# Kernel optimization log

Hardware: AMD Instinct MI355X
Metric: run time of the kernel (lower is better)

Reference implementation:

```python
import jax, jax.numpy as jnp
import numpy as np

D, H, KV, HD, F = 2048, 16, 4, 128, 5632
WIN, NG = 512, 64          # sliding window size, num global tokens
EPS = 1e-6
KEEP_ATTN = 1.0 - 0.82     # Ramanujan sparsity on attention projections
KEEP_FFN = 1.0 - 0.88      # Ramanujan sparsity on FFN projections


def _mask_w(key, shape, keep):
    """Fixed structured-sparse weight: dense init * binary keep-mask."""
    k1, k2 = jax.random.split(key)
    w = jax.random.normal(k1, shape, dtype=jnp.float32) * (shape[0] ** -0.5)
    m = (jax.random.uniform(k2, shape) < keep).astype(jnp.float32)
    return w * m


def setup_inputs() -> dict:
    key = jax.random.key(0)
    ks = jax.random.split(key, 8)
    x = jax.random.normal(ks[0], (1, 2048, D), dtype=jnp.float32)
    return {
        "x": x,
        "g_attn": jnp.ones((D,), jnp.float32),   # RMSNorm weight (attn)
        "g_ffn": jnp.ones((D,), jnp.float32),    # RMSNorm weight (ffn)
        "wq": _mask_w(ks[1], (D, H * HD), KEEP_ATTN),
        "wk": _mask_w(ks[2], (D, KV * HD), KEEP_ATTN),
        "wv": _mask_w(ks[3], (D, KV * HD), KEEP_ATTN),
        "wo": _mask_w(ks[4], (H * HD, D), KEEP_ATTN),
        "w1": _mask_w(ks[5], (D, F), KEEP_FFN),   # SwiGLU gate proj
        "w3": _mask_w(ks[6], (D, F), KEEP_FFN),   # SwiGLU up proj
        "w2": _mask_w(ks[7], (F, D), KEEP_FFN),   # SwiGLU down proj
    }


def _rmsnorm(x, g):
    return x * jax.lax.rsqrt(jnp.mean(x * x, axis=-1, keepdims=True) + EPS) * g


def _qknorm(t):  # RMS-normalize over head_dim (QK-Normalization)
    return t * jax.lax.rsqrt(jnp.mean(t * t, axis=-1, keepdims=True) + EPS)


def reference(x, g_attn, g_ffn, wq, wk, wv, wo, w1, w2, w3):
    B, S, _ = x.shape
    # --- attention sub-block: x = x + SlidingWindowGQA(RMSNorm(x)) ---
    h = _rmsnorm(x, g_attn)
    q = h @ wq
    q = q.reshape(B, S, H, HD)
    k = (h @ wk).reshape(B, S, KV, HD)
    v = (h @ wv).reshape(B, S, KV, HD)
    q, k = _qknorm(q), _qknorm(k)
    rep = H // KV
    k = jnp.repeat(k, rep, axis=2)  # [B,S,H,HD]
    v = jnp.repeat(v, rep, axis=2)
    scores = jnp.einsum("bihd,bjhd->bhij", q, k) * (HD ** -0.5)
    # causal + (sliding window OR global row OR global column)
    i = jnp.arange(S)[:, None]
    j = jnp.arange(S)[None, :]
    allowed = (j <= i) & (((i - j) < WIN) | (j < NG) | (i < NG))
    scores = jnp.where(allowed[None, None], scores, jnp.float32(-1e30))
    attn = jax.nn.softmax(scores, axis=-1)
    o = jnp.einsum("bhij,bjhd->bihd", attn, v).reshape(B, S, H * HD)
    x = x + o @ wo
    # --- FFN sub-block: x = x + SparseSwiGLU(RMSNorm(x)) ---
    h2 = _rmsnorm(x, g_ffn)
    ffn = (jax.nn.silu(h2 @ w1) * (h2 @ w3)) @ w2
    return x + ffn
```

## Files before the change

kernel.cpp:

```cpp
#include <hip/hip_runtime.h>
#include <hip/hip_bf16.h>
#include <stdint.h>

typedef _Float16 fp16_t;
typedef __attribute__((ext_vector_type(8))) _Float16 fp16x8;
typedef __attribute__((ext_vector_type(4))) _Float16 fp16x4;
typedef __attribute__((ext_vector_type(4))) float f32x4;

#define WIN 512
#define NG 64

__device__ __forceinline__ void gload16(const void* g, void* l) {
    __builtin_amdgcn_global_load_lds((const __attribute__((address_space(1))) void*)g,
                                     (__attribute__((address_space(3))) void*)l, 16, 0, 0);
}

__global__ __launch_bounds__(256) void transpose_f2b(const float* __restrict__ in,
                                                     fp16_t* __restrict__ out,
                                                     int R, int C) {
    __shared__ fp16_t t[64][68];
    int tid = threadIdx.x;
    int tx = tid & 15, ty = tid >> 4;
    int c0 = blockIdx.x * 64, r0 = blockIdx.y * 64;
#pragma unroll
    for (int j = 0; j < 4; ++j) {
        int r = ty + j * 16;
        float4 v = *(const float4*)&in[(size_t)(r0 + r) * C + c0 + tx * 4];
        t[tx * 4 + 0][r] = (fp16_t)v.x;
        t[tx * 4 + 1][r] = (fp16_t)v.y;
        t[tx * 4 + 2][r] = (fp16_t)v.z;
        t[tx * 4 + 3][r] = (fp16_t)v.w;
    }
    __syncthreads();
#pragma unroll
    for (int jj = 0; jj < 4; ++jj) {
        int c_l = ty + jj * 16;
        int r_l = tx * 4;
        *(fp16x4*)&out[(size_t)(c0 + c_l) * R + r0 + r_l] = *(const fp16x4*)&t[c_l][r_l];
    }
}

__global__ void transpose_b2b(const fp16_t* __restrict__ in, fp16_t* __restrict__ out,
                              int R, int C, int in_ld, int in_off) {
    __shared__ fp16_t t[32][33];
    int tx = threadIdx.x, ty = threadIdx.y;
    int c0 = blockIdx.x * 32, r0 = blockIdx.y * 32;
#pragma unroll
    for (int j = 0; j < 32; j += 8)
        t[ty + j][tx] = in[(size_t)(r0 + ty + j) * in_ld + in_off + c0 + tx];
    __syncthreads();
#pragma unroll
    for (int j = 0; j < 32; j += 8)
        out[(size_t)(c0 + ty + j) * R + r0 + tx] = t[tx][ty + j];
}

__global__ __launch_bounds__(256) void rmsnorm_kernel(const float* __restrict__ in,
                                                      const float* __restrict__ g,
                                                      fp16_t* __restrict__ out) {
    int row = blockIdx.x;
    int tid = threadIdx.x;
    const float4* rp = (const float4*)(in + (size_t)row * 2048);
    float4 v0 = rp[tid], v1 = rp[tid + 256];
    float ss = v0.x * v0.x + v0.y * v0.y + v0.z * v0.z + v0.w * v0.w +
               v1.x * v1.x + v1.y * v1.y + v1.z * v1.z + v1.w * v1.w;
#pragma unroll
    for (int m = 1; m < 64; m <<= 1) ss += __shfl_xor(ss, m);
    __shared__ float red[4];
    if ((tid & 63) == 0) red[tid >> 6] = ss;
    __syncthreads();
    ss = red[0] + red[1] + red[2] + red[3];
    float sc = rsqrtf(ss * (1.0f / 2048.0f) + 1e-6f);
    const float4* gp = (const float4*)g;
    float4 g0 = gp[tid], g1 = gp[tid + 256];
    fp16x4 o0 = { (fp16_t)(v0.x * sc * g0.x), (fp16_t)(v0.y * sc * g0.y),
                  (fp16_t)(v0.z * sc * g0.z), (fp16_t)(v0.w * sc * g0.w) };
    fp16x4 o1 = { (fp16_t)(v1.x * sc * g1.x), (fp16_t)(v1.y * sc * g1.y),
                  (fp16_t)(v1.z * sc * g1.z), (fp16_t)(v1.w * sc * g1.w) };
    *(fp16x4*)(out + (size_t)row * 2048 + tid * 4) = o0;
    *(fp16x4*)(out + (size_t)row * 2048 + 1024 + tid * 4) = o1;
}

__global__ __launch_bounds__(256) void rmsnorm_add2(const float* __restrict__ xin,
                                                    const float* __restrict__ p0,
                                                    const float* __restrict__ p1,
                                                    const float* __restrict__ g,
                                                    float* __restrict__ x1out,
                                                    fp16_t* __restrict__ hout) {
    int row = blockIdx.x;
    int tid = threadIdx.x;
    size_t base = (size_t)row * 2048;
    const float4* xp = (const float4*)(xin + base);
    const float4* ap = (const float4*)(p0 + base);
    const float4* bp = (const float4*)(p1 + base);
    float4 v0 = xp[tid], v1 = xp[tid + 256];
    float4 a0 = ap[tid], a1 = ap[tid + 256];
    float4 b0 = bp[tid], b1 = bp[tid + 256];
    v0.x += a0.x + b0.x; v0.y += a0.y + b0.y; v0.z += a0.z + b0.z; v0.w += a0.w + b0.w;
    v1.x += a1.x + b1.x; v1.y += a1.y + b1.y; v1.z += a1.z + b1.z; v1.w += a1.w + b1.w;
    float ss = v0.x * v0.x + v0.y * v0.y + v0.z * v0.z + v0.w * v0.w +
               v1.x * v1.x + v1.y * v1.y + v1.z * v1.z + v1.w * v1.w;
#pragma unroll
    for (int m = 1; m < 64; m <<= 1) ss += __shfl_xor(ss, m);
    __shared__ float red[4];
    if ((tid & 63) == 0) red[tid >> 6] = ss;
    __syncthreads();
    ss = red[0] + red[1] + red[2] + red[3];
    float sc = rsqrtf(ss * (1.0f / 2048.0f) + 1e-6f);
    ((float4*)(x1out + base))[tid] = v0;
    ((float4*)(x1out + base))[tid + 256] = v1;
    const float4* gp = (const float4*)g;
    float4 g0 = gp[tid], g1 = gp[tid + 256];
    fp16x4 o0 = { (fp16_t)(v0.x * sc * g0.x), (fp16_t)(v0.y * sc * g0.y),
                  (fp16_t)(v0.z * sc * g0.z), (fp16_t)(v0.w * sc * g0.w) };
    fp16x4 o1 = { (fp16_t)(v1.x * sc * g1.x), (fp16_t)(v1.y * sc * g1.y),
                  (fp16_t)(v1.z * sc * g1.z), (fp16_t)(v1.w * sc * g1.w) };
    *(fp16x4*)(hout + base + tid * 4) = o0;
    *(fp16x4*)(hout + base + 1024 + tid * 4) = o1;
}

__global__ __launch_bounds__(256) void final_add2(float* __restrict__ out,
                                                  const float* __restrict__ p0,
                                                  const float* __restrict__ p1) {
    size_t i = (size_t)blockIdx.x * 256 + threadIdx.x;
    float4 o = ((const float4*)out)[i];
    float4 a = ((const float4*)p0)[i];
    float4 b = ((const float4*)p1)[i];
    o.x += a.x + b.x; o.y += a.y + b.y; o.z += a.z + b.z; o.w += a.w + b.w;
    ((float4*)out)[i] = o;
}

__global__ __launch_bounds__(256) void qknorm_kernel(fp16_t* __restrict__ qkv) {
    int seg = blockIdx.x * 4 + (threadIdx.x >> 6);
    int lane = threadIdx.x & 63;
    int row = seg / 20, hs = seg % 20;
    int col0 = hs < 16 ? hs * 128 : 2048 + (hs - 16) * 128;
    fp16_t* p = qkv + (size_t)row * 3072 + col0 + lane * 2;
    float a = (float)p[0], b = (float)p[1];
    float ss = a * a + b * b;
#pragma unroll
    for (int m = 1; m < 64; m <<= 1) ss += __shfl_xor(ss, m);
    float sc = rsqrtf(ss * (1.0f / 128.0f) + 1e-6f);
    if (hs < 16) sc *= 0.08838834764831843f;
    p[0] = (fp16_t)(a * sc);
    p[1] = (fp16_t)(b * sc);
}

__global__ __launch_bounds__(256) void silu_mul_kernel(fp16_t* __restrict__ u1,
                                                       const fp16_t* __restrict__ u3) {
    size_t idx = ((size_t)blockIdx.x * 256 + threadIdx.x) * 8;
    fp16x8 a = *(const fp16x8*)(u1 + idx);
    fp16x8 b = *(const fp16x8*)(u3 + idx);
    fp16x8 r;
#pragma unroll
    for (int e = 0; e < 8; ++e) {
        float xg = (float)a[e], xu = (float)b[e];
        float s = xg / (1.0f + __expf(-xg));
        r[e] = (fp16_t)(s * xu);
    }
    *(fp16x8*)(u1 + idx) = r;
}

#define BM 128
#define BN 128
#define BKK 64

struct GemmCore {
    int tid, lane, wid, lo, hi, wr, wc;
    int arow[4], ascb[4];
    __device__ __forceinline__ void init(int t) {
        tid = t; lane = t & 63; wid = t >> 6;
        lo = lane & 15; hi = lane >> 4;
        wr = (wid >> 1) * 64; wc = (wid & 1) * 64;
#pragma unroll
        for (int p = 0; p < 4; ++p) {
            int idx = (wid * 4 + p) * 64 + lane;
            int row = idx >> 3;
            int cb = (idx & 7) << 4;
            arow[p] = row;
            ascb[p] = cb ^ ((row & 7) << 4);
        }
    }
    __device__ __forceinline__ void stage(char* buf, const fp16_t* A, const fp16_t* Bt,
                                          int brow, int bcol, int lda, int ldb, int kb) {
        char* As = buf;
        char* Bs = buf + 16384;
#pragma unroll
        for (int p = 0; p < 4; ++p) {
            int ci = wid * 4 + p;
            gload16((const char*)A + ((size_t)(brow + arow[p]) * lda + kb) * 2 + ascb[p],
                    As + ci * 1024);
            gload16((const char*)Bt + ((size_t)(bcol + arow[p]) * ldb + kb) * 2 + ascb[p],
                    Bs + ci * 1024);
        }
    }
    __device__ __forceinline__ void compute(const char* buf, f32x4 (&acc)[4][4]) {
        const char* As = buf;
        const char* Bs = buf + 16384;
#pragma unroll
        for (int kc = 0; kc < 2; ++kc) {
            fp16x8 af[4], bfr[4];
            int boff = kc * 64 + hi * 16;
#pragma unroll
            for (int m = 0; m < 4; ++m) {
                int row = wr + m * 16 + lo;
                af[m] = *(const fp16x8*)(As + row * 128 + (boff ^ ((row & 7) << 4)));
            }
#pragma unroll
            for (int n = 0; n < 4; ++n) {
                int row = wc + n * 16 + lo;
                bfr[n] = *(const fp16x8*)(Bs + row * 128 + (boff ^ ((row & 7) << 4)));
            }
#pragma unroll
            for (int m = 0; m < 4; ++m)
#pragma unroll
                for (int n = 0; n < 4; ++n)
                    acc[m][n] = __builtin_amdgcn_mfma_f32_16x16x32_f16(af[m], bfr[n], acc[m][n], 0, 0, 0);
        }
    }
};

template <int EPI>
__global__ __launch_bounds__(256, 2) void gemm_bt(const fp16_t* __restrict__ A,
                                                  const fp16_t* __restrict__ Bt,
                                                  void* __restrict__ Cout,
                                                  const float* __restrict__ resid,
                                                  int M, int N, int K,
                                                  int lda, int ldb, int ksplit) {
    __shared__ __align__(16) char smem[2][32768];
    GemmCore g;
    g.init(threadIdx.x);
    int brow = blockIdx.y * BM, bcol = blockIdx.x * BN;

    int Kloc = K / ksplit;
    int kbase0 = blockIdx.z * Kloc;
    int nK = Kloc / BKK;

    f32x4 acc[4][4] = {};
    g.stage(smem[0], A, Bt, brow, bcol, lda, ldb, kbase0);
    __syncthreads();
    for (int kt = 0; kt < nK; ++kt) {
        if (kt + 1 < nK) g.stage(smem[(kt + 1) & 1], A, Bt, brow, bcol, lda, ldb,
                                 kbase0 + (kt + 1) * BKK);
        g.compute(smem[kt & 1], acc);
        __syncthreads();
    }

#pragma unroll
    for (int m = 0; m < 4; ++m) {
        int grow0 = brow + g.wr + m * 16 + g.hi * 4;
#pragma unroll
        for (int n = 0; n < 4; ++n) {
            int gcol = bcol + g.wc + n * 16 + g.lo;
#pragma unroll
            for (int r = 0; r < 4; ++r) {
                size_t gidx = (size_t)(grow0 + r) * N + gcol;
                float v = acc[m][n][r];
                if (EPI == 0) {
                    ((fp16_t*)Cout)[gidx] = (fp16_t)v;
                } else if (EPI == 1) {
                    ((float*)Cout)[gidx] = v + resid[gidx];
                } else {
                    ((float*)Cout)[(size_t)blockIdx.z * M * N + gidx] = v;
                }
            }
        }
    }
}

__global__ __launch_bounds__(256, 2) void gemm_bt_dual(const fp16_t* __restrict__ A,
                                                       const fp16_t* __restrict__ Bt0,
                                                       const fp16_t* __restrict__ Bt1,
                                                       fp16_t* __restrict__ C0,
                                                       fp16_t* __restrict__ C1,
                                                       int M, int N, int K) {
    __shared__ __align__(16) char smem[2][32768];
    GemmCore g;
    g.init(threadIdx.x);
    const fp16_t* Bt = blockIdx.z ? Bt1 : Bt0;
    fp16_t* Cout = blockIdx.z ? C1 : C0;
    int brow = blockIdx.y * BM, bcol = blockIdx.x * BN;
    int nK = K / BKK;

    f32x4 acc[4][4] = {};
    g.stage(smem[0], A, Bt, brow, bcol, K, K, 0);
    __syncthreads();
    for (int kt = 0; kt < nK; ++kt) {
        if (kt + 1 < nK) g.stage(smem[(kt + 1) & 1], A, Bt, brow, bcol, K, K, (kt + 1) * BKK);
        g.compute(smem[kt & 1], acc);
        __syncthreads();
    }

#pragma unroll
    for (int m = 0; m < 4; ++m) {
        int grow0 = brow + g.wr + m * 16 + g.hi * 4;
#pragma unroll
        for (int n = 0; n < 4; ++n) {
            int gcol = bcol + g.wc + n * 16 + g.lo;
#pragma unroll
            for (int r = 0; r < 4; ++r)
                Cout[(size_t)(grow0 + r) * N + gcol] = (fp16_t)acc[m][n][r];
        }
    }
}

__global__ __launch_bounds__(256, 2) void attn_kernel(const fp16_t* __restrict__ qkv,
                                                      const fp16_t* __restrict__ vT,
                                                      fp16_t* __restrict__ o) {
    __shared__ __align__(16) char smem[16384 + 16384 + 4 * 2304];
    char* Ks = smem;
    char* VTs = smem + 16384;
    char* Ps = smem + 32768;

    int t = blockIdx.x, qh = blockIdx.y;
    int kvh = qh >> 2;
    int qs = t * 64;
    int tid = threadIdx.x, lane = tid & 63, wid = tid >> 6;
    int lo = lane & 15, hi = lane >> 4;

    fp16x8 qf[4];
    {
        const fp16_t* qptr = qkv + (size_t)(qs + wid * 16 + lo) * 3072 + qh * 128 + hi * 8;
#pragma unroll
        for (int kc = 0; kc < 4; ++kc) qf[kc] = *(const fp16x8*)(qptr + kc * 32);
    }

    f32x4 oacc[8] = {};
    float m_r[4], l_r[4];
#pragma unroll
    for (int r = 0; r < 4; ++r) { m_r[r] = -1e30f; l_r[r] = 0.0f; }

    int lot = qs - (WIN - 1);
    int jt_lo = lot <= 0 ? 0 : (lot >> 6);
    int nt = (jt_lo > 0) ? (t - jt_lo + 2) : (t + 1);

    for (int ti = 0; ti < nt; ++ti) {
        int jt = (jt_lo > 0) ? (ti == 0 ? 0 : jt_lo + ti - 1) : ti;
        int js = jt * 64;
        __syncthreads();
#pragma unroll
        for (int p = 0; p < 4; ++p) {
            int ci = wid * 4 + p;
            int idx = ci * 64 + lane;
            int krow = idx >> 4;
            int kcb = (idx & 15) << 4;
            int kscb = kcb ^ ((krow & 7) << 4);
            gload16((const char*)qkv + ((size_t)(js + krow) * 3072 + 2048 + kvh * 128) * 2 + kscb,
                    Ks + ci * 1024);
            int vrow = idx >> 3;
            int vcb = (idx & 7) << 4;
            int vscb = vcb ^ ((vrow & 7) << 4);
            gload16((const char*)vT + ((size_t)(kvh * 128 + vrow) * 2048 + js) * 2 + vscb,
                    VTs + ci * 1024);
        }
        __syncthreads();

        f32x4 s[4] = {};
#pragma unroll
        for (int kc = 0; kc < 4; ++kc) {
#pragma unroll
            for (int jc = 0; jc < 4; ++jc) {
                int row = jc * 16 + lo;
                fp16x8 kf = *(const fp16x8*)(Ks + row * 256 + ((kc * 64 + hi * 16) ^ ((row & 7) << 4)));
                s[jc] = __builtin_amdgcn_mfma_f32_16x16x32_f16(qf[kc], kf, s[jc], 0, 0, 0);
            }
        }

        float mt[4] = { -1e30f, -1e30f, -1e30f, -1e30f };
#pragma unroll
        for (int jc = 0; jc < 4; ++jc) {
            int j = js + jc * 16 + lo;
#pragma unroll
            for (int r = 0; r < 4; ++r) {
                int i = qs + wid * 16 + hi * 4 + r;
                bool ok = (j <= i) && (((i - j) < WIN) || (j < NG) || (i < NG));
                float sv = ok ? s[jc][r] : -1e30f;
                s[jc][r] = sv;
                mt[r] = fmaxf(mt[r], sv);
            }
        }
#pragma unroll
        for (int m2 = 1; m2 <= 8; m2 <<= 1)
#pragma unroll
            for (int r = 0; r < 4; ++r) mt[r] = fmaxf(mt[r], __shfl_xor(mt[r], m2));
        float sf[4], psum[4];
#pragma unroll
        for (int r = 0; r < 4; ++r) {
            float mn = fmaxf(m_r[r], mt[r]);
            sf[r] = __expf(m_r[r] - mn);
            m_r[r] = mn;
            psum[r] = 0.0f;
        }
#pragma unroll
        for (int jc = 0; jc < 4; ++jc)
#pragma unroll
            for (int r = 0; r < 4; ++r) {
                float p = __expf(s[jc][r] - m_r[r]);
                s[jc][r] = p;
                psum[r] += p;
            }
#pragma unroll
        for (int m2 = 1; m2 <= 8; m2 <<= 1)
#pragma unroll
            for (int r = 0; r < 4; ++r) psum[r] += __shfl_xor(psum[r], m2);
#pragma unroll
        for (int r = 0; r < 4; ++r) l_r[r] = l_r[r] * sf[r] + psum[r];
#pragma unroll
        for (int nc = 0; nc < 8; ++nc)
#pragma unroll
            for (int r = 0; r < 4; ++r) oacc[nc][r] *= sf[r];

        char* Pb = Ps + wid * 2304;
#pragma unroll
        for (int jc = 0; jc < 4; ++jc)
#pragma unroll
            for (int r = 0; r < 4; ++r)
                *(fp16_t*)(Pb + (hi * 4 + r) * 144 + (jc * 16 + lo) * 2) = (fp16_t)s[jc][r];
        fp16x8 pa[2];
#pragma unroll
        for (int jc2 = 0; jc2 < 2; ++jc2)
            pa[jc2] = *(const fp16x8*)(Pb + lo * 144 + jc2 * 64 + hi * 16);

#pragma unroll
        for (int jc2 = 0; jc2 < 2; ++jc2)
#pragma unroll
            for (int nc = 0; nc < 8; ++nc) {
                int row = nc * 16 + lo;
                fp16x8 vf = *(const fp16x8*)(VTs + row * 128 + ((jc2 * 64 + hi * 16) ^ ((row & 7) << 4)));
                oacc[nc] = __builtin_amdgcn_mfma_f32_16x16x32_f16(pa[jc2], vf, oacc[nc], 0, 0, 0);
            }
    }

#pragma unroll
    for (int r = 0; r < 4; ++r) {
        float inv = 1.0f / l_r[r];
        int orow = qs + wid * 16 + hi * 4 + r;
#pragma unroll
        for (int nc = 0; nc < 8; ++nc)
            o[(size_t)orow * 2048 + qh * 128 + nc * 16 + lo] = (fp16_t)(oacc[nc][r] * inv);
    }
}

extern "C" void kernel_launch(void* const* d_in, const int* in_sizes, int n_in,
                              void* d_out, int out_size, void* d_ws, size_t ws_size,
                              hipStream_t stream) {
    const float* x = (const float*)d_in[0];
    const float* g_attn = (const float*)d_in[1];
    const float* g_ffn = (const float*)d_in[2];
    const float* wq = (const float*)d_in[3];
    const float* wk = (const float*)d_in[4];
    const float* wv = (const float*)d_in[5];
    const float* wo = (const float*)d_in[6];
    const float* w1 = (const float*)d_in[7];
    const float* w3 = (const float*)d_in[8];
    const float* w2 = (const float*)d_in[9];
    float* out = (float*)d_out;

    char* ws = (char*)d_ws;
    size_t off = 0;
    auto alloc = [&](size_t bytes) {
        char* p = ws + off;
        off += (bytes + 255) & ~(size_t)255;
        return p;
    };
    fp16_t* hbuf  = (fp16_t*)alloc(2048ull * 2048 * 2);
    fp16_t* wqkvT = (fp16_t*)alloc(3072ull * 2048 * 2);
    fp16_t* vTb   = (fp16_t*)alloc(512ull * 2048 * 2);
    fp16_t* qkv   = (fp16_t*)alloc(2048ull * 3072 * 2);
    fp16_t* u1    = (fp16_t*)alloc(2048ull * 5632 * 2);
    fp16_t* u3    = (fp16_t*)alloc(2048ull * 5632 * 2);
    float*  part  = (float*)alloc(2ull * 2048 * 2048 * 4);
    fp16_t* wbigT = (fp16_t*)alloc(5632ull * 2048 * 2);
    if (off > ws_size) {
        hipMemsetAsync(d_out, 0, (size_t)out_size * 4, stream);
        return;
    }
    float* part1 = part + 2048ull * 2048;
    fp16_t* w3T = hbuf;

    transpose_f2b<<<dim3(32, 32), 256, 0, stream>>>(wq, wqkvT, 2048, 2048);
    transpose_f2b<<<dim3(8, 32), 256, 0, stream>>>(wk, wqkvT + 2048ull * 2048, 2048, 512);
    transpose_f2b<<<dim3(8, 32), 256, 0, stream>>>(wv, wqkvT + 2560ull * 2048, 2048, 512);
    rmsnorm_kernel<<<2048, 256, 0, stream>>>(x, g_attn, hbuf);
    gemm_bt<0><<<dim3(24, 16, 1), 256, 0, stream>>>(hbuf, wqkvT, qkv, nullptr,
                                                    2048, 3072, 2048, 2048, 2048, 1);
    qknorm_kernel<<<10240, 256, 0, stream>>>(qkv);
    transpose_b2b<<<dim3(16, 64), dim3(32, 8), 0, stream>>>(qkv, vTb, 2048, 512, 3072, 2560);
    attn_kernel<<<dim3(32, 16), 256, 0, stream>>>(qkv, vTb, hbuf);
    transpose_f2b<<<dim3(32, 32), 256, 0, stream>>>(wo, wqkvT, 2048, 2048);
    gemm_bt<2><<<dim3(16, 16, 2), 256, 0, stream>>>(hbuf, wqkvT, part, nullptr,
                                                    2048, 2048, 2048, 2048, 2048, 2);
    rmsnorm_add2<<<2048, 256, 0, stream>>>(x, part, part1, g_ffn, out, qkv);
    transpose_f2b<<<dim3(88, 32), 256, 0, stream>>>(w1, wbigT, 2048, 5632);
    transpose_f2b<<<dim3(88, 32), 256, 0, stream>>>(w3, w3T, 2048, 5632);
    gemm_bt_dual<<<dim3(44, 16, 2), 256, 0, stream>>>(qkv, wbigT, w3T, u1, u3,
                                                      2048, 5632, 2048);
    silu_mul_kernel<<<5632, 256, 0, stream>>>(u1, u3);
    transpose_f2b<<<dim3(32, 88), 256, 0, stream>>>(w2, wbigT, 5632, 2048);
    gemm_bt<2><<<dim3(16, 16, 2), 256, 0, stream>>>(u1, wbigT, part, nullptr,
                                                    2048, 2048, 5632, 5632, 5632, 2);
    final_add2<<<4096, 256, 0, stream>>>(out, part, part1);
}
```

Baseline: 337.8 us.

## Fuse QK-norm into QKV GEMM epilogue, SwiGLU into dual GEMM, merge transposes

Moves the per-head QK RMS normalization into the QKV GEMM epilogue, with a cross-wave reduction through shared memory, so the separate qknorm pass over qkv goes away. Computes the gate and up projections sequentially in one block with two accumulator sets and applies SiLU*mul in the epilogue, which removes the u1/u3 round trip and the silu kernel. Merges the weight transpose launches and changes the transpose's shared-memory write pattern. The fused SwiGLU kernel holds twice the accumulators, which can hurt occupancy, and it launches half as many blocks, each doing twice the work.

```diff
diff --git a/kernel.cpp b/kernel.cpp
--- a/kernel.cpp
+++ b/kernel.cpp
@@ -5,6 +5,7 @@
 typedef _Float16 fp16_t;
 typedef __attribute__((ext_vector_type(8))) _Float16 fp16x8;
 typedef __attribute__((ext_vector_type(4))) _Float16 fp16x4;
+typedef __attribute__((ext_vector_type(2))) _Float16 fp16x2;
 typedef __attribute__((ext_vector_type(4))) float f32x4;
 
 #define WIN 512
@@ -15,29 +16,53 @@
                                      (__attribute__((address_space(3))) void*)l, 16, 0, 0);
 }
 
-__global__ __launch_bounds__(256) void transpose_f2b(const float* __restrict__ in,
-                                                     fp16_t* __restrict__ out,
-                                                     int R, int C) {
-    __shared__ fp16_t t[64][68];
+__device__ __forceinline__ void tr_tile(const float* __restrict__ src, int C, int srow, int scol,
+                                        fp16_t* __restrict__ out, int R, int orow) {
+    __shared__ fp16_t t[64][66];
     int tid = threadIdx.x;
     int tx = tid & 15, ty = tid >> 4;
-    int c0 = blockIdx.x * 64, r0 = blockIdx.y * 64;
 #pragma unroll
     for (int j = 0; j < 4; ++j) {
         int r = ty + j * 16;
-        float4 v = *(const float4*)&in[(size_t)(r0 + r) * C + c0 + tx * 4];
-        t[tx * 4 + 0][r] = (fp16_t)v.x;
-        t[tx * 4 + 1][r] = (fp16_t)v.y;
-        t[tx * 4 + 2][r] = (fp16_t)v.z;
-        t[tx * 4 + 3][r] = (fp16_t)v.w;
+        float4 v = *(const float4*)&src[(size_t)(srow + r) * C + scol + tx * 4];
+        fp16x2 a = { (fp16_t)v.x, (fp16_t)v.y };
+        fp16x2 b = { (fp16_t)v.z, (fp16_t)v.w };
+        *(fp16x2*)&t[r][tx * 4] = a;
+        *(fp16x2*)&t[r][tx * 4 + 2] = b;
     }
     __syncthreads();
 #pragma unroll
     for (int jj = 0; jj < 4; ++jj) {
-        int c_l = ty + jj * 16;
-        int r_l = tx * 4;
-        *(fp16x4*)&out[(size_t)(c0 + c_l) * R + r0 + r_l] = *(const fp16x4*)&t[c_l][r_l];
-    }
+        int c = ty + jj * 16;
+        fp16x4 o = { t[tx * 4 + 0][c], t[tx * 4 + 1][c], t[tx * 4 + 2][c], t[tx * 4 + 3][c] };
+        *(fp16x4*)&out[(size_t)(orow + c) * R + srow + tx * 4] = o;
+    }
+}
+
+__global__ __launch_bounds__(256) void transpose_qkv3(const float* __restrict__ wq,
+                                                      const float* __restrict__ wk,
+                                                      const float* __restrict__ wv,
+                                                      fp16_t* __restrict__ out) {
+    int n0 = blockIdx.x * 64, k0 = blockIdx.y * 64;
+    const float* src; int C, c0;
+    if (n0 < 2048)      { src = wq; C = 2048; c0 = n0; }
+    else if (n0 < 2560) { src = wk; C = 512;  c0 = n0 - 2048; }
+    else                { src = wv; C = 512;  c0 = n0 - 2560; }
+    tr_tile(src, C, k0, c0, out, 2048, n0);
+}
+
+__global__ __launch_bounds__(256) void transpose_w13(const float* __restrict__ w1,
+                                                     const float* __restrict__ w3,
+                                                     fp16_t* __restrict__ o1,
+                                                     fp16_t* __restrict__ o3) {
+    const float* src = blockIdx.z ? w3 : w1;
+    fp16_t* out = blockIdx.z ? o3 : o1;
+    tr_tile(src, 5632, blockIdx.y * 64, blockIdx.x * 64, out, 2048, blockIdx.x * 64);
+}
+
+__global__ __launch_bounds__(256) void transpose_one(const float* __restrict__ src,
+                                                     fp16_t* __restrict__ out, int R, int C) {
+    tr_tile(src, C, blockIdx.y * 64, blockIdx.x * 64, out, R, blockIdx.x * 64);
 }
 
 __global__ void transpose_b2b(const fp16_t* __restrict__ in, fp16_t* __restrict__ out,
@@ -129,37 +154,6 @@
     ((float4*)out)[i] = o;
 }
 
-__global__ __launch_bounds__(256) void qknorm_kernel(fp16_t* __restrict__ qkv) {
-    int seg = blockIdx.x * 4 + (threadIdx.x >> 6);
-    int lane = threadIdx.x & 63;
-    int row = seg / 20, hs = seg % 20;
-    int col0 = hs < 16 ? hs * 128 : 2048 + (hs - 16) * 128;
-    fp16_t* p = qkv + (size_t)row * 3072 + col0 + lane * 2;
-    float a = (float)p[0], b = (float)p[1];
-    float ss = a * a + b * b;
-#pragma unroll
-    for (int m = 1; m < 64; m <<= 1) ss += __shfl_xor(ss, m);
-    float sc = rsqrtf(ss * (1.0f / 128.0f) + 1e-6f);
-    if (hs < 16) sc *= 0.08838834764831843f;
-    p[0] = (fp16_t)(a * sc);
-    p[1] = (fp16_t)(b * sc);
-}
-
-__global__ __launch_bounds__(256) void silu_mul_kernel(fp16_t* __restrict__ u1,
-                                                       const fp16_t* __restrict__ u3) {
-    size_t idx = ((size_t)blockIdx.x * 256 + threadIdx.x) * 8;
-    fp16x8 a = *(const fp16x8*)(u1 + idx);
-    fp16x8 b = *(const fp16x8*)(u3 + idx);
-    fp16x8 r;
-#pragma unroll
-    for (int e = 0; e < 8; ++e) {
-        float xg = (float)a[e], xu = (float)b[e];
-        float s = xg / (1.0f + __expf(-xg));
-        r[e] = (fp16_t)(s * xu);
-    }
-    *(fp16x8*)(u1 + idx) = r;
-}
-
 #define BM 128
 #define BN 128
 #define BKK 64
@@ -245,6 +239,36 @@
         __syncthreads();
     }
 
+    if (EPI == 3) {
+        if (blockIdx.x < 20) {
+            float* sq = (float*)smem;
+            bool isq = blockIdx.x < 16;
+#pragma unroll
+            for (int m = 0; m < 4; ++m)
+#pragma unroll
+                for (int r = 0; r < 4; ++r) {
+                    float s = 0.f;
+#pragma unroll
+                    for (int n = 0; n < 4; ++n) s += acc[m][n][r] * acc[m][n][r];
+                    s += __shfl_xor(s, 1); s += __shfl_xor(s, 2);
+                    s += __shfl_xor(s, 4); s += __shfl_xor(s, 8);
+                    if (g.lo == 0) sq[g.wid * 64 + m * 16 + g.hi * 4 + r] = s;
+                }
+            __syncthreads();
+#pragma unroll
+            for (int m = 0; m < 4; ++m)
+#pragma unroll
+                for (int r = 0; r < 4; ++r) {
+                    int rl = m * 16 + g.hi * 4 + r;
+                    float tot = sq[g.wid * 64 + rl] + sq[(g.wid ^ 1) * 64 + rl];
+                    float sc = rsqrtf(tot * (1.0f / 128.0f) + 1e-6f);
+                    if (isq) sc *= 0.08838834764831843f;
+#pragma unroll
+                    for (int n = 0; n < 4; ++n) acc[m][n] [r] *= sc;
+                }
+        }
+    }
+
 #pragma unroll
     for (int m = 0; m < 4; ++m) {
         int grow0 = brow + g.wr + m * 16 + g.hi * 4;
@@ -255,7 +279,7 @@
             for (int r = 0; r < 4; ++r) {
                 size_t gidx = (size_t)(grow0 + r) * N + gcol;
                 float v = acc[m][n][r];
-                if (EPI == 0) {
+                if (EPI == 0 || EPI == 3) {
                     ((fp16_t*)Cout)[gidx] = (fp16_t)v;
                 } else if (EPI == 1) {
                     ((float*)Cout)[gidx] = v + resid[gidx];
@@ -267,26 +291,29 @@
     }
 }
 
-__global__ __launch_bounds__(256, 2) void gemm_bt_dual(const fp16_t* __restrict__ A,
-                                                       const fp16_t* __restrict__ Bt0,
-                                                       const fp16_t* __restrict__ Bt1,
-                                                       fp16_t* __restrict__ C0,
-                                                       fp16_t* __restrict__ C1,
-                                                       int M, int N, int K) {
+__global__ __launch_bounds__(256, 2) void gemm_u1u3_fused(const fp16_t* __restrict__ A,
+                                                          const fp16_t* __restrict__ Bt1,
+                                                          const fp16_t* __restrict__ Bt3,
+                                                          fp16_t* __restrict__ G,
+                                                          int M, int N, int K) {
     __shared__ __align__(16) char smem[2][32768];
     GemmCore g;
     g.init(threadIdx.x);
-    const fp16_t* Bt = blockIdx.z ? Bt1 : Bt0;
-    fp16_t* Cout = blockIdx.z ? C1 : C0;
     int brow = blockIdx.y * BM, bcol = blockIdx.x * BN;
     int nK = K / BKK;
 
-    f32x4 acc[4][4] = {};
-    g.stage(smem[0], A, Bt, brow, bcol, K, K, 0);
+    f32x4 acc1[4][4] = {}, acc3[4][4] = {};
+    g.stage(smem[0], A, Bt1, brow, bcol, K, K, 0);
     __syncthreads();
     for (int kt = 0; kt < nK; ++kt) {
-        if (kt + 1 < nK) g.stage(smem[(kt + 1) & 1], A, Bt, brow, bcol, K, K, (kt + 1) * BKK);
-        g.compute(smem[kt & 1], acc);
+        if (kt + 1 < nK) g.stage(smem[(kt + 1) & 1], A, Bt1, brow, bcol, K, K, (kt + 1) * BKK);
+        else             g.stage(smem[(kt + 1) & 1], A, Bt3, brow, bcol, K, K, 0);
+        g.compute(smem[kt & 1], acc1);
+        __syncthreads();
+    }
+    for (int kt = 0; kt < nK; ++kt) {
+        if (kt + 1 < nK) g.stage(smem[(nK + kt + 1) & 1], A, Bt3, brow, bcol, K, K, (kt + 1) * BKK);
+        g.compute(smem[(nK + kt) & 1], acc3);
         __syncthreads();
     }
 
@@ -297,8 +324,11 @@
         for (int n = 0; n < 4; ++n) {
             int gcol = bcol + g.wc + n * 16 + g.lo;
 #pragma unroll
-            for (int r = 0; r < 4; ++r)
-                Cout[(size_t)(grow0 + r) * N + gcol] = (fp16_t)acc[m][n][r];
+            for (int r = 0; r < 4; ++r) {
+                float u = acc1[m][n][r];
+                float val = (u / (1.0f + __expf(-u))) * acc3[m][n][r];
+                G[(size_t)(grow0 + r) * N + gcol] = (fp16_t)val;
+            }
         }
     }
 }
@@ -466,8 +496,7 @@
     fp16_t* wqkvT = (fp16_t*)alloc(3072ull * 2048 * 2);
     fp16_t* vTb   = (fp16_t*)alloc(512ull * 2048 * 2);
     fp16_t* qkv   = (fp16_t*)alloc(2048ull * 3072 * 2);
-    fp16_t* u1    = (fp16_t*)alloc(2048ull * 5632 * 2);
-    fp16_t* u3    = (fp16_t*)alloc(2048ull * 5632 * 2);
+    fp16_t* gbuf  = (fp16_t*)alloc(2048ull * 5632 * 2);
     float*  part  = (float*)alloc(2ull * 2048 * 2048 * 4);
     fp16_t* wbigT = (fp16_t*)alloc(5632ull * 2048 * 2);
     if (off > ws_size) {
@@ -477,26 +506,20 @@
     float* part1 = part + 2048ull * 2048;
     fp16_t* w3T = hbuf;
 
-    transpose_f2b<<<dim3(32, 32), 256, 0, stream>>>(wq, wqkvT, 2048, 2048);
-    transpose_f2b<<<dim3(8, 32), 256, 0, stream>>>(wk, wqkvT + 2048ull * 2048, 2048, 512);
-    transpose_f2b<<<dim3(8, 32), 256, 0, stream>>>(wv, wqkvT + 2560ull * 2048, 2048, 512);
+    transpose_qkv3<<<dim3(48, 32), 256, 0, stream>>>(wq, wk, wv, wqkvT);
     rmsnorm_kernel<<<2048, 256, 0, stream>>>(x, g_attn, hbuf);
-    gemm_bt<0><<<dim3(24, 16, 1), 256, 0, stream>>>(hbuf, wqkvT, qkv, nullptr,
+    gemm_bt<3><<<dim3(24, 16, 1), 256, 0, stream>>>(hbuf, wqkvT, qkv, nullptr,
                                                     2048, 3072, 2048, 2048, 2048, 1);
-    qknorm_kernel<<<10240, 256, 0, stream>>>(qkv);
     transpose_b2b<<<dim3(16, 64), dim3(32, 8), 0, stream>>>(qkv, vTb, 2048, 512, 3072, 2560);
     attn_kernel<<<dim3(32, 16), 256, 0, stream>>>(qkv, vTb, hbuf);
-    transpose_f2b<<<dim3(32, 32), 256, 0, stream>>>(wo, wqkvT, 2048, 2048);
+    transpose_one<<<dim3(32, 32), 256, 0, stream>>>(wo, wqkvT, 2048, 2048);
     gemm_bt<2><<<dim3(16, 16, 2), 256, 0, stream>>>(hbuf, wqkvT, part, nullptr,
                                                     2048, 2048, 2048, 2048, 2048, 2);
     rmsnorm_add2<<<2048, 256, 0, stream>>>(x, part, part1, g_ffn, out, qkv);
-    transpose_f2b<<<dim3(88, 32), 256, 0, stream>>>(w1, wbigT, 2048, 5632);
-    transpose_f2b<<<dim3(88, 32), 256, 0, stream>>>(w3, w3T, 2048, 5632);
-    gemm_bt_dual<<<dim3(44, 16, 2), 256, 0, stream>>>(qkv, wbigT, w3T, u1, u3,
-                                                      2048, 5632, 2048);
-    silu_mul_kernel<<<5632, 256, 0, stream>>>(u1, u3);
-    transpose_f2b<<<dim3(32, 88), 256, 0, stream>>>(w2, wbigT, 5632, 2048);
-    gemm_bt<2><<<dim3(16, 16, 2), 256, 0, stream>>>(u1, wbigT, part, nullptr,
+    transpose_w13<<<dim3(88, 32, 2), 256, 0, stream>>>(w1, w3, wbigT, w3T);
+    gemm_u1u3_fused<<<dim3(44, 16), 256, 0, stream>>>(qkv, wbigT, w3T, gbuf, 2048, 5632, 2048);
+    transpose_one<<<dim3(32, 88), 256, 0, stream>>>(w2, wbigT, 5632, 2048);
+    gemm_bt<2><<<dim3(16, 16, 2), 256, 0, stream>>>(gbuf, wbigT, part, nullptr,
                                                     2048, 2048, 5632, 5632, 5632, 2);
     final_add2<<<4096, 256, 0, stream>>>(out, part, part1);
 }
```

After: 323.5 us. -4.2%, faster.
